# Kernel optimization log

Hardware: AMD Instinct MI355X
Metric: run time of the kernel (lower is better)

Reference implementation:

```python
import jax, jax.numpy as jnp
import numpy as np

N, E, IN_FEATS, HID, HEADS = 50000, 800000, 256, 32, 8
NEG_SLOPE = 0.2


def _init_params(key):
    ks = jax.random.split(key, 12)
    def lin(k, fi, fo):
        return jax.random.normal(k, (fi, fo), jnp.float32) * (1.0 / np.sqrt(fi))
    p = {}
    # layer 0: in_feats -> HID x HEADS
    p['W0'] = lin(ks[0], IN_FEATS, HEADS * HID)
    p['al0'] = jax.random.normal(ks[1], (HEADS, HID), jnp.float32) * 0.1
    p['ar0'] = jax.random.normal(ks[2], (HEADS, HID), jnp.float32) * 0.1
    p['b0'] = jnp.zeros((HEADS * HID,), jnp.float32)
    # layer 1: HID*HEADS -> HID x HEADS
    p['W1'] = lin(ks[3], HEADS * HID, HEADS * HID)
    p['al1'] = jax.random.normal(ks[4], (HEADS, HID), jnp.float32) * 0.1
    p['ar1'] = jax.random.normal(ks[5], (HEADS, HID), jnp.float32) * 0.1
    p['b1'] = jnp.zeros((HEADS * HID,), jnp.float32)
    # layer 2 (final): HID*HEADS -> HID x 1 head, no activation
    p['W2'] = lin(ks[6], HEADS * HID, HID)
    p['al2'] = jax.random.normal(ks[7], (1, HID), jnp.float32) * 0.1
    p['ar2'] = jax.random.normal(ks[8], (1, HID), jnp.float32) * 0.1
    p['b2'] = jnp.zeros((HID,), jnp.float32)
    return p


def setup_inputs() -> dict:
    key = jax.random.key(0)
    k1, k2, k3, kp = jax.random.split(key, 4)
    inp = {
        'features': jax.random.normal(k1, (N, IN_FEATS), jnp.float32),
        'src': jax.random.randint(k2, (E,), 0, N, jnp.int32),
        'dst': jax.random.randint(k3, (E,), 0, N, jnp.int32),
    }
    inp.update(_init_params(kp))
    return inp


def _gat_layer(x, src, dst, W, al, ar, b, heads, act):
    n = x.shape[0]
    d = W.shape[1] // heads
    feat = (x @ W).reshape(n, heads, d)           # [N,H,D]
    el = jnp.sum(feat * al, axis=-1)              # [N,H]
    er = jnp.sum(feat * ar, axis=-1)              # [N,H]
    e = jax.nn.leaky_relu(el[src] + er[dst], NEG_SLOPE)   # [E,H]
    # segment softmax over destination neighborhoods
    emax = jax.ops.segment_max(e, dst, num_segments=n)
    ex = jnp.exp(e - emax[dst])
    denom = jax.ops.segment_sum(ex, dst, num_segments=n)
    a = ex / (denom[dst] + 1e-9)                  # [E,H]
    msg = feat[src] * a[:, :, None]               # [E,H,D]
    out = jax.ops.segment_sum(msg, dst, num_segments=n)   # [N,H,D]
    out = out + b.reshape(1, heads, d)
    return act(out) if act is not None else out


def reference(features, src, dst, W0, al0, ar0, b0, W1, al1, ar1, b1, W2, al2, ar2, b2):
    h = _gat_layer(features, src, dst, W0, al0, ar0, b0, HEADS, jax.nn.elu)
    h = h.reshape(h.shape[0], -1)
    h = _gat_layer(h, src, dst, W1, al1, ar1, b1, HEADS, jax.nn.elu)
    h = h.reshape(h.shape[0], -1)
    h = _gat_layer(h, src, dst, W2, al2, ar2, b2, 1, None)   # [N,1,D]
    return h.mean(axis=1)                                    # [N,D]
```

## Files before the change

### kernel.cpp

```cpp
#include <hip/hip_runtime.h>

typedef unsigned short u16;
typedef unsigned int   u32;
typedef __attribute__((ext_vector_type(8))) short  short8;
typedef __attribute__((ext_vector_type(4))) float  f32x4;
typedef __attribute__((ext_vector_type(2))) float  f32x2;
typedef __attribute__((ext_vector_type(2))) unsigned int u32v2;
typedef __attribute__((ext_vector_type(4))) unsigned int u32v4;

#define NN 50000
#define NE 800000

__device__ __forceinline__ float bf2f(u16 b) { return __uint_as_float(((u32)b) << 16); }
__device__ __forceinline__ float bflo(u32 p) { return __uint_as_float(p << 16); }
__device__ __forceinline__ float bfhi(u32 p) { return __uint_as_float(p & 0xffff0000u); }
__device__ __forceinline__ u16 f2bf(float f) {
    u32 u = __float_as_uint(f);
    u32 r = u + 0x7fffu + ((u >> 16) & 1u);
    return (u16)(r >> 16);
}
__device__ __forceinline__ float lexp(float v) {
    v = fmaxf(v, 0.2f * v);
    return __expf(fminf(v, 60.f));
}

struct DetectArgs { const u32* p[13]; int nw[13]; };

__global__ __launch_bounds__(256) void k_detect(DetectArgs a, int* flags) {
    __shared__ int sh[256], sz[256];
    int j = blockIdx.x;
    const u32* x = a.p[j];
    int n = a.nw[j];
    int t = threadIdx.x;
    int hits = 0, nz = 0;
    for (int i = t; i < n; i += 256) {
        u32 w = x[i];
        if (w) {
            ++nz;
            u32 e = (w >> 7) & 0xffu;
            if (e >= 100 && e <= 150) ++hits;
        }
    }
    sh[t] = hits; sz[t] = nz;
    __syncthreads();
    for (int ofs = 128; ofs > 0; ofs >>= 1) {
        if (t < ofs) { sh[t] += sh[t + ofs]; sz[t] += sz[t + ofs]; }
        __syncthreads();
    }
    if (t == 0) flags[j] = (sz[0] == 0) ? 2 : ((sh[0] * 2 >= sz[0]) ? 0 : 1);
}

struct ConvArgs { const void* s[9]; float* d[9]; int n[9]; int fi[9]; };

__global__ void k_convert(ConvArgs a, const int* __restrict__ flags) {
    int j = blockIdx.y;
    int i = blockIdx.x * 256 + threadIdx.x;
    if (i >= a.n[j]) return;
    int fl = flags[a.fi[j]];
    float v = 0.f;
    if (fl == 1) v = ((const float*)a.s[j])[i];
    else if (fl == 0) v = bf2f(((const u16*)a.s[j])[i]);
    a.d[j][i] = v;
}

__global__ void k_wpack(const void* __restrict__ Wsrc, const int* __restrict__ flags,
                        int fidx, int N, u16* __restrict__ Wp, int nchunks) {
    int id = blockIdx.x * 256 + threadIdx.x;
    if (id >= nchunks) return;
    int L = id & 63, kt = (id >> 6) & 7, nt = id >> 9;
    int col = nt * 16 + (L & 15);
    int krow = kt * 32 + ((L >> 4) & 3) * 8;
    bool isf32 = (flags[fidx] == 1);
#pragma unroll
    for (int j = 0; j < 8; ++j) {
        int s = (krow + j) * N + col;
        Wp[id * 8 + j] = isf32 ? f2bf(((const float*)Wsrc)[s]) : ((const u16*)Wsrc)[s];
    }
}

__global__ void k_hist(const int* __restrict__ dst, int* __restrict__ deg, int E) {
    int e = blockIdx.x * 256 + threadIdx.x;
    if (e < E) atomicAdd(&deg[dst[e]], 1);
}

__global__ __launch_bounds__(256) void k_scan_partial(const int* __restrict__ deg,
                                                      int* __restrict__ bsum, int n) {
    __shared__ int red[256];
    int t = threadIdx.x;
    int i = blockIdx.x * 256 + t;
    red[t] = (i < n) ? deg[i] : 0;
    __syncthreads();
    for (int ofs = 128; ofs > 0; ofs >>= 1) {
        if (t < ofs) red[t] += red[t + ofs];
        __syncthreads();
    }
    if (t == 0) bsum[blockIdx.x] = red[0];
}

__global__ __launch_bounds__(256) void k_scan_bsum(int* __restrict__ bsum, int nb) {
    __shared__ int s[256];
    int t = threadIdx.x;
    int v = (t < nb) ? bsum[t] : 0;
    s[t] = v;
    __syncthreads();
    for (int ofs = 1; ofs < 256; ofs <<= 1) {
        int x = (t >= ofs) ? s[t - ofs] : 0;
        __syncthreads();
        s[t] += x;
        __syncthreads();
    }
    if (t < nb) bsum[t] = s[t] - v;
}

__global__ __launch_bounds__(256) void k_scan_final(const int* __restrict__ deg,
                                                    const int* __restrict__ bsum,
                                                    int* __restrict__ rowptr,
                                                    int* __restrict__ cursor, int n) {
    __shared__ int s[256];
    int t = threadIdx.x;
    int i = blockIdx.x * 256 + t;
    int v = (i < n) ? deg[i] : 0;
    s[t] = v;
    __syncthreads();
    for (int ofs = 1; ofs < 256; ofs <<= 1) {
        int x = (t >= ofs) ? s[t - ofs] : 0;
        __syncthreads();
        s[t] += x;
        __syncthreads();
    }
    int excl = bsum[blockIdx.x] + s[t] - v;
    if (i < n) {
        rowptr[i] = excl;
        cursor[i] = excl;
        if (i == n - 1) rowptr[n] = excl + v;
    }
}

__global__ void k_scatter(const int* __restrict__ src, const int* __restrict__ dst,
                          int* __restrict__ cursor, int* __restrict__ csr_src, int E) {
    int e = blockIdx.x * 256 + threadIdx.x;
    if (e >= E) return;
    int p = atomicAdd(&cursor[dst[e]], 1);
    csr_src[p] = src[e];
}

__global__ __launch_bounds__(256) void k_gemm_mfma(const void* __restrict__ Xv,
                                                   const int* __restrict__ xflag,
                                                   const u16* __restrict__ Wp,
                                                   u16* __restrict__ OUT, int nrows) {
    __shared__ u16 As[64 * 256];
    const int t = threadIdx.x;
    const int w = t >> 6, L = t & 63;
    const int quad = (L >> 4) & 3;
    const int r0 = blockIdx.x * 64;
    const int nb = blockIdx.y * 8;
    const bool xf32 = (xflag != nullptr) && (*xflag == 1);

    short8* Asv = (short8*)As;
    short8 zero = {0, 0, 0, 0, 0, 0, 0, 0};
#pragma unroll
    for (int i = 0; i < 8; ++i) {
        int g = i * 256 + t;
        int row = g >> 5, cc = g & 31;
        int r = r0 + row;
        short8 val = zero;
        if (r < nrows) {
            if (xf32) {
                const f32x4* Xf4 = (const f32x4*)Xv;
                f32x4 lo = Xf4[(size_t)r * 64 + cc * 2];
                f32x4 hi = Xf4[(size_t)r * 64 + cc * 2 + 1];
                val[0] = (short)f2bf(lo[0]); val[1] = (short)f2bf(lo[1]);
                val[2] = (short)f2bf(lo[2]); val[3] = (short)f2bf(lo[3]);
                val[4] = (short)f2bf(hi[0]); val[5] = (short)f2bf(hi[1]);
                val[6] = (short)f2bf(hi[2]); val[7] = (short)f2bf(hi[3]);
            } else {
                val = ((const short8*)Xv)[(size_t)r * 32 + cc];
            }
        }
        Asv[cc * 64 + (row ^ (cc & 7))] = val;
    }

    const short8* Wv = (const short8*)Wp;
    short8 bf[2][8];
#pragma unroll
    for (int jn = 0; jn < 2; ++jn) {
        int nt = nb + w + jn * 4;
#pragma unroll
        for (int kt = 0; kt < 8; ++kt) bf[jn][kt] = Wv[(nt * 8 + kt) * 64 + L];
    }
    __syncthreads();

    f32x4 acc[4][2];
#pragma unroll
    for (int mi = 0; mi < 4; ++mi)
#pragma unroll
        for (int jn = 0; jn < 2; ++jn) acc[mi][jn] = (f32x4){0.f, 0.f, 0.f, 0.f};

#pragma unroll
    for (int kt = 0; kt < 8; ++kt) {
        const int ccr = kt * 4 + quad;
#pragma unroll
        for (int mi = 0; mi < 4; ++mi) {
            short8 af = Asv[ccr * 64 + ((mi * 16 + (L & 15)) ^ (ccr & 7))];
            acc[mi][0] = __builtin_amdgcn_mfma_f32_16x16x32_bf16(af, bf[0][kt], acc[mi][0], 0, 0, 0);
            acc[mi][1] = __builtin_amdgcn_mfma_f32_16x16x32_bf16(af, bf[1][kt], acc[mi][1], 0, 0, 0);
        }
    }

    const int colbase = blockIdx.y * 128;
#pragma unroll
    for (int mi = 0; mi < 4; ++mi) {
        int rb = r0 + mi * 16 + quad * 4;
#pragma unroll
        for (int jn = 0; jn < 2; ++jn) {
            int c = colbase + (w + jn * 4) * 16 + (L & 15);
#pragma unroll
            for (int reg = 0; reg < 4; ++reg) {
                int r = rb + reg;
                if (r < nrows) OUT[(size_t)r * 256 + c] = f2bf(acc[mi][jn][reg]);
            }
        }
    }
}

__global__ __launch_bounds__(256) void k_gemm_mfma32(const u16* __restrict__ Xb,
                                                     const u16* __restrict__ Wp,
                                                     u16* __restrict__ OUT, int nrows) {
    __shared__ u16 As[128 * 256];
    const int t = threadIdx.x;
    const int w = t >> 6, L = t & 63;
    const int quad = (L >> 4) & 3;
    const int r0 = blockIdx.x * 128;
    const int mh = (w >> 1) * 64, nt = w & 1;

    const short8* Xv = (const short8*)Xb;
    short8* Asv = (short8*)As;
    short8 zero = {0, 0, 0, 0, 0, 0, 0, 0};
#pragma unroll
    for (int i = 0; i < 16; ++i) {
        int g = i * 256 + t;
        int row = g >> 5, cc = g & 31;
        int r = r0 + row;
        Asv[cc * 128 + (row ^ (cc & 7))] = (r < nrows) ? Xv[(size_t)r * 32 + cc] : zero;
    }

    const short8* Wv = (const short8*)Wp;
    short8 bf[8];
#pragma unroll
    for (int kt = 0; kt < 8; ++kt) bf[kt] = Wv[(nt * 8 + kt) * 64 + L];
    __syncthreads();

    f32x4 acc[4];
#pragma unroll
    for (int mi = 0; mi < 4; ++mi) acc[mi] = (f32x4){0.f, 0.f, 0.f, 0.f};

#pragma unroll
    for (int kt = 0; kt < 8; ++kt) {
        const int ccr = kt * 4 + quad;
#pragma unroll
        for (int mi = 0; mi < 4; ++mi) {
            short8 af = Asv[ccr * 128 + ((mh + mi * 16 + (L & 15)) ^ (ccr & 7))];
            acc[mi] = __builtin_amdgcn_mfma_f32_16x16x32_bf16(af, bf[kt], acc[mi], 0, 0, 0);
        }
    }

#pragma unroll
    for (int mi = 0; mi < 4; ++mi) {
        int rb = r0 + mh + mi * 16 + quad * 4;
        int c = nt * 16 + (L & 15);
#pragma unroll
        for (int reg = 0; reg < 4; ++reg) {
            int r = rb + reg;
            if (r < nrows) OUT[(size_t)r * 32 + c] = f2bf(acc[mi][reg]);
        }
    }
}

__global__ void k_elr8(const u16* __restrict__ featb, const float* __restrict__ al,
                       const float* __restrict__ ar, float* __restrict__ el,
                       float* __restrict__ er, int n) {
    int idx = blockIdx.x * 256 + threadIdx.x;
    if (idx >= n * 8) return;
    int node = idx >> 3, h = idx & 7;
    const u32v4* fu = (const u32v4*)((const u32*)featb + (size_t)node * 128 + h * 16);
    const float* A = al + h * 32;
    const float* B = ar + h * 32;
    float sl = 0.f, sr = 0.f;
#pragma unroll
    for (int j = 0; j < 4; ++j) {
        u32v4 w4 = fu[j];
#pragma unroll
        for (int k = 0; k < 4; ++k) {
            u32 w = (k == 0) ? w4.x : (k == 1) ? w4.y : (k == 2) ? w4.z : w4.w;
            float f0 = bflo(w), f1 = bfhi(w);
            int c = j * 8 + k * 2;
            sl += f0 * A[c] + f1 * A[c + 1];
            sr += f0 * B[c] + f1 * B[c + 1];
        }
    }
    el[idx] = sl;
    er[idx] = sr;
}

__global__ void k_elr1(const u16* __restrict__ featb, const float* __restrict__ al,
                       const float* __restrict__ ar, float* __restrict__ el,
                       float* __restrict__ er, int n) {
    int node = blockIdx.x * 256 + threadIdx.x;
    if (node >= n) return;
    const u32v4* fu = (const u32v4*)((const u32*)featb + (size_t)node * 16);
    float sl = 0.f, sr = 0.f;
#pragma unroll
    for (int j = 0; j < 4; ++j) {
        u32v4 w4 = fu[j];
#pragma unroll
        for (int k = 0; k < 4; ++k) {
            u32 w = (k == 0) ? w4.x : (k == 1) ? w4.y : (k == 2) ? w4.z : w4.w;
            float f0 = bflo(w), f1 = bfhi(w);
            int c = j * 8 + k * 2;
            sl += f0 * al[c] + f1 * al[c + 1];
            sr += f0 * ar[c] + f1 * ar[c + 1];
        }
    }
    el[node] = sl;
    er[node] = sr;
}

__global__ __launch_bounds__(256) void k_gather8(const int* __restrict__ rowptr,
                                                 const int* __restrict__ csr_src,
                                                 const float* __restrict__ el,
                                                 const float* __restrict__ er,
                                                 const u32v2* __restrict__ featb4,
                                                 const float* __restrict__ bias,
                                                 u32v2* __restrict__ xout4) {
    __shared__ __align__(16) float sAL[4][2][64];
    __shared__ __align__(16) int   sSL[4][2][8];
    const int t = threadIdx.x;
    const int wv = t >> 6;
    const int q = t & 63;
    const int d = blockIdx.x * 4 + wv;
    const int eL = q >> 3, hL = q & 7;
    const int b = rowptr[d], e = rowptr[d + 1];
    const int deg = e - b;
    const int nch = (deg + 7) >> 3;
    const float erA = er[d * 8 + hL];

    float (*AL)[64] = sAL[wv];
    int (*SL)[8] = sSL[wv];

    float a0 = 0.f, a1 = 0.f, a2 = 0.f, a3 = 0.f;
    float partial = 0.f;

    u32v2 fw[8], fw2[8];
    int csrP = 0, ncP = 0;
    float elP = 0.f;

    if (nch > 0) {
        const int nc0 = deg < 8 ? deg : 8;
        const int i0 = eL < nc0 ? eL : nc0 - 1;
        const int s0 = csr_src[b + i0];
        if (nch > 1) {
            const int r1 = deg - 8;
            ncP = r1 < 8 ? r1 : 8;
            const int i1 = eL < ncP ? eL : ncP - 1;
            csrP = csr_src[b + 8 + i1];
        }
        const float el0 = el[s0 * 8 + hL];
        if (hL == 0) SL[0][eL] = s0;
        const int4 sv0 = *(const int4*)&SL[0][0];
        const int4 sv1 = *(const int4*)&SL[0][4];
        fw[0] = featb4[sv0.x * 64 + q];
        fw[1] = featb4[sv0.y * 64 + q];
        fw[2] = featb4[sv0.z * 64 + q];
        fw[3] = featb4[sv0.w * 64 + q];
        fw[4] = featb4[sv1.x * 64 + q];
        fw[5] = featb4[sv1.y * 64 + q];
        fw[6] = featb4[sv1.z * 64 + q];
        fw[7] = featb4[sv1.w * 64 + q];
        const float ex0 = (eL < nc0) ? lexp(el0 + erA) : 0.f;
        partial += ex0;
        AL[0][hL * 8 + eL] = ex0;
        if (nch > 1) elP = el[csrP * 8 + hL];
    }

    for (int c = 0; c < nch; ++c) {
        const int cur = c & 1, nxt = cur ^ 1;

        int csrF = 0, ncF = 0;
        if (c + 2 < nch) {
            const int r2 = deg - (c + 2) * 8;
            ncF = r2 < 8 ? r2 : 8;
            const int i2 = eL < ncF ? eL : ncF - 1;
            csrF = csr_src[b + (c + 2) * 8 + i2];
        }

        if (c + 1 < nch) {
            if (hL == 0) SL[nxt][eL] = csrP;
            const int4 sv0 = *(const int4*)&SL[nxt][0];
            const int4 sv1 = *(const int4*)&SL[nxt][4];
            fw2[0] = featb4[sv0.x * 64 + q];
            fw2[1] = featb4[sv0.y * 64 + q];
            fw2[2] = featb4[sv0.z * 64 + q];
            fw2[3] = featb4[sv0.w * 64 + q];
            fw2[4] = featb4[sv1.x * 64 + q];
            fw2[5] = featb4[sv1.y * 64 + q];
            fw2[6] = featb4[sv1.z * 64 + q];
            fw2[7] = featb4[sv1.w * 64 + q];
            const float exN = (eL < ncP) ? lexp(elP + erA) : 0.f;
            partial += exN;
            AL[nxt][hL * 8 + eL] = exN;
        }

        const int h8 = (q >> 3) * 8;
        const f32x4 A0 = *(const f32x4*)&AL[cur][h8];
        const f32x4 A1 = *(const f32x4*)&AL[cur][h8 + 4];

        if (c + 2 < nch) elP = el[csrF * 8 + hL];

#define GAT_EDGE(i, axv) { const u32v2 w_ = fw[i]; \
        a0 += bflo(w_.x) * (axv); a1 += bfhi(w_.x) * (axv); \
        a2 += bflo(w_.y) * (axv); a3 += bfhi(w_.y) * (axv); }
        GAT_EDGE(0, A0[0]) GAT_EDGE(1, A0[1]) GAT_EDGE(2, A0[2]) GAT_EDGE(3, A0[3])
        GAT_EDGE(4, A1[0]) GAT_EDGE(5, A1[1]) GAT_EDGE(6, A1[2]) GAT_EDGE(7, A1[3])
#undef GAT_EDGE

#pragma unroll
        for (int i = 0; i < 8; ++i) fw[i] = fw2[i];
        csrP = csrF;
        ncP = ncF;
    }

    float v = partial;
    v += __shfl_xor(v, 8);
    v += __shfl_xor(v, 16);
    v += __shfl_xor(v, 32);
    const float ssd = __shfl(v, q >> 3);

    const float rd = 1.f / (ssd + 1e-9f);
    const float4 bb = *(const float4*)&bias[4 * q];
    float v0 = a0 * rd + bb.x;
    float v1 = a1 * rd + bb.y;
    float v2 = a2 * rd + bb.z;
    float v3 = a3 * rd + bb.w;
    v0 = v0 > 0.f ? v0 : expm1f(v0);
    v1 = v1 > 0.f ? v1 : expm1f(v1);
    v2 = v2 > 0.f ? v2 : expm1f(v2);
    v3 = v3 > 0.f ? v3 : expm1f(v3);
    u32v2 o;
    o.x = (u32)f2bf(v0) | ((u32)f2bf(v1) << 16);
    o.y = (u32)f2bf(v2) | ((u32)f2bf(v3) << 16);
    xout4[(size_t)d * 64 + q] = o;
}

__global__ __launch_bounds__(256) void k_gather1(const int* __restrict__ rowptr,
                                                 const int* __restrict__ csr_src,
                                                 const float* __restrict__ el,
                                                 const float* __restrict__ er,
                                                 const u32* __restrict__ featb2,
                                                 const float* __restrict__ bias,
                                                 void* __restrict__ out,
                                                 const int* __restrict__ flag, int n) {
    int t = threadIdx.x;
    int d = blockIdx.x * 16 + (t >> 4);
    int q = t & 15;
    if (d >= n) return;
    int b = rowptr[d], e = rowptr[d + 1];
    float erd = er[d];
    float a0 = 0.f, a1 = 0.f, ssum = 0.f;
    int p = b;
    for (; p + 4 <= e; p += 4) {
        int s0 = csr_src[p], s1 = csr_src[p + 1], s2 = csr_src[p + 2], s3 = csr_src[p + 3];
        float e0 = lexp(el[s0] + erd);
        float e1 = lexp(el[s1] + erd);
        float e2 = lexp(el[s2] + erd);
        float e3 = lexp(el[s3] + erd);
        u32 w0 = featb2[(size_t)s0 * 16 + q];
        u32 w1 = featb2[(size_t)s1 * 16 + q];
        u32 w2 = featb2[(size_t)s2 * 16 + q];
        u32 w3 = featb2[(size_t)s3 * 16 + q];
        a0 += bflo(w0) * e0; a1 += bfhi(w0) * e0;
        a0 += bflo(w1) * e1; a1 += bfhi(w1) * e1;
        a0 += bflo(w2) * e2; a1 += bfhi(w2) * e2;
        a0 += bflo(w3) * e3; a1 += bfhi(w3) * e3;
        ssum += (e0 + e1) + (e2 + e3);
    }
    for (; p < e; ++p) {
        int s = csr_src[p];
        float ev = lexp(el[s] + erd);
        u32 w = featb2[(size_t)s * 16 + q];
        a0 += bflo(w) * ev;
        a1 += bfhi(w) * ev;
        ssum += ev;
    }
    float rd = 1.f / (ssum + 1e-9f);
    float v0 = a0 * rd + bias[2 * q];
    float v1 = a1 * rd + bias[2 * q + 1];
    if (*flag == 1) {
        f32x2 o = {v0, v1};
        ((f32x2*)out)[(size_t)d * 16 + q] = o;
    } else {
        ((u32*)out)[(size_t)d * 16 + q] = (u32)f2bf(v0) | ((u32)f2bf(v1) << 16);
    }
}

extern "C" void kernel_launch(void* const* d_in, const int* in_sizes, int n_in,
                              void* d_out, int out_size, void* d_ws, size_t ws_size,
                              hipStream_t stream) {
    const void* features = d_in[0];
    const int* src = (const int*)d_in[1];
    const int* dst = (const int*)d_in[2];

    char* ws = (char*)d_ws;
    size_t off = 0;
    auto carve = [&](size_t bytes) -> void* {
        void* p = ws + off;
        off = (off + bytes + 255) & ~(size_t)255;
        return p;
    };
    int*   flags = (int*)carve(64);
    float* pconv = (float*)carve(2048 * 4);
    u16*   Wp0 = (u16*)carve(65536 * 2);
    u16*   Wp1 = (u16*)carve(65536 * 2);
    u16*   Wp2 = (u16*)carve(8192 * 2);
    u16*   Xb    = (u16*)carve((size_t)NN * 256 * 2);
    u16*   featb = (u16*)carve((size_t)NN * 256 * 2);
    float* el   = (float*)carve((size_t)NN * 8 * 4);
    float* er   = (float*)carve((size_t)NN * 8 * 4);
    int*   deg     = (int*)carve((size_t)NN * 4);
    int*   cursor  = (int*)carve((size_t)NN * 4);
    int*   rowptr  = (int*)carve((size_t)(NN + 1) * 4);
    int*   bsum    = (int*)carve(256 * 4);
    int*   csr_src = (int*)carve((size_t)NE * 4);
    if (off > ws_size) return;

    const int N = NN, E = NE;
    const int nscan = (N + 255) / 256;

    DetectArgs da;
    const int din_idx[13] = {0, 3, 4, 5, 6, 7, 8, 9, 10, 11, 12, 13, 14};
    for (int j = 0; j < 13; ++j) {
        da.p[j] = (const u32*)d_in[din_idx[j]];
        int nw = in_sizes[din_idx[j]] / 2;
        da.nw[j] = nw > 512 ? 512 : nw;
    }
    k_detect<<<13, 256, 0, stream>>>(da, flags);

    ConvArgs ca;
    const int psl[9] = {4, 5, 6, 8, 9, 10, 12, 13, 14};
    const int pfl[9] = {2, 3, 4, 6, 7, 8, 10, 11, 12};
    float* dsts[9];
    {
        size_t o = 0;
        for (int j = 0; j < 9; ++j) {
            dsts[j] = pconv + o;
            o += (size_t)in_sizes[psl[j]];
        }
    }
    for (int j = 0; j < 9; ++j) {
        ca.s[j] = d_in[psl[j]];
        ca.d[j] = dsts[j];
        ca.n[j] = in_sizes[psl[j]];
        ca.fi[j] = pfl[j];
    }
    k_convert<<<dim3(1, 9), 256, 0, stream>>>(ca, flags);
    float* al0f = dsts[0]; float* ar0f = dsts[1]; float* b0f = dsts[2];
    float* al1f = dsts[3]; float* ar1f = dsts[4]; float* b1f = dsts[5];
    float* al2f = dsts[6]; float* ar2f = dsts[7]; float* b2f = dsts[8];

    k_wpack<<<32, 256, 0, stream>>>(d_in[3],  flags, 1, 256, Wp0, 8192);
    k_wpack<<<32, 256, 0, stream>>>(d_in[7],  flags, 5, 256, Wp1, 8192);
    k_wpack<<<4,  256, 0, stream>>>(d_in[11], flags, 9, 32,  Wp2, 1024);

    hipMemsetAsync(deg, 0, (size_t)N * 4, stream);
    k_hist<<<(E + 255) / 256, 256, 0, stream>>>(dst, deg, E);
    k_scan_partial<<<nscan, 256, 0, stream>>>(deg, bsum, N);
    k_scan_bsum<<<1, 256, 0, stream>>>(bsum, nscan);
    k_scan_final<<<nscan, 256, 0, stream>>>(deg, bsum, rowptr, cursor, N);
    k_scatter<<<(E + 255) / 256, 256, 0, stream>>>(src, dst, cursor, csr_src, E);

    const dim3 ggrid((N + 63) / 64, 2);

    k_gemm_mfma<<<ggrid, 256, 0, stream>>>(features, flags, Wp0, featb, N);
    k_elr8<<<(N * 8 + 255) / 256, 256, 0, stream>>>(featb, al0f, ar0f, el, er, N);
    k_gather8<<<N / 4, 256, 0, stream>>>(rowptr, csr_src, el, er,
                                         (const u32v2*)featb, b0f, (u32v2*)Xb);

    k_gemm_mfma<<<ggrid, 256, 0, stream>>>(Xb, nullptr, Wp1, featb, N);
    k_elr8<<<(N * 8 + 255) / 256, 256, 0, stream>>>(featb, al1f, ar1f, el, er, N);
    k_gather8<<<N / 4, 256, 0, stream>>>(rowptr, csr_src, el, er,
                                         (const u32v2*)featb, b1f, (u32v2*)Xb);

    k_gemm_mfma32<<<(N + 127) / 128, 256, 0, stream>>>(Xb, Wp2, featb, N);
    k_elr1<<<(N + 255) / 256, 256, 0, stream>>>(featb, al2f, ar2f, el, er, N);
    k_gather1<<<(N + 15) / 16, 256, 0, stream>>>(rowptr, csr_src, el, er,
                                                 (const u32*)featb, b2f,
                                                 d_out, flags, N);
}
```

Measured before the change: 447.3 us.

## Merge prep kernels into one launch and widen GEMM blocks to full width

Combines the dtype-detect, parameter-convert and weight-pack kernels into a single prep kernel in which each block runs its own format detection, removing four launches and the flag dependency between them. Separately, the layer-0/1 GEMM now uses 512-thread blocks that cover all 256 output columns, so each 64-row A tile is loaded into shared memory once instead of twice. The cost is redundant detect work in every prep block and a larger block that may lower occupancy.

Result: faster. 418.4 us (-6.5%).

```diff
diff --git a/kernel.cpp b/kernel.cpp
--- a/kernel.cpp
+++ b/kernel.cpp
@@ -24,13 +24,7 @@
     return __expf(fminf(v, 60.f));
 }
 
-struct DetectArgs { const u32* p[13]; int nw[13]; };
-
-__global__ __launch_bounds__(256) void k_detect(DetectArgs a, int* flags) {
-    __shared__ int sh[256], sz[256];
-    int j = blockIdx.x;
-    const u32* x = a.p[j];
-    int n = a.nw[j];
+__device__ __forceinline__ int block_detect(const u32* x, int n, int* sh, int* sz) {
     int t = threadIdx.x;
     int hits = 0, nz = 0;
     for (int i = t; i < n; i += 256) {
@@ -47,34 +41,54 @@
         if (t < ofs) { sh[t] += sh[t + ofs]; sz[t] += sz[t + ofs]; }
         __syncthreads();
     }
-    if (t == 0) flags[j] = (sz[0] == 0) ? 2 : ((sh[0] * 2 >= sz[0]) ? 0 : 1);
-}
-
-struct ConvArgs { const void* s[9]; float* d[9]; int n[9]; int fi[9]; };
-
-__global__ void k_convert(ConvArgs a, const int* __restrict__ flags) {
-    int j = blockIdx.y;
-    int i = blockIdx.x * 256 + threadIdx.x;
-    if (i >= a.n[j]) return;
-    int fl = flags[a.fi[j]];
-    float v = 0.f;
-    if (fl == 1) v = ((const float*)a.s[j])[i];
-    else if (fl == 0) v = bf2f(((const u16*)a.s[j])[i]);
-    a.d[j][i] = v;
-}
-
-__global__ void k_wpack(const void* __restrict__ Wsrc, const int* __restrict__ flags,
-                        int fidx, int N, u16* __restrict__ Wp, int nchunks) {
-    int id = blockIdx.x * 256 + threadIdx.x;
-    if (id >= nchunks) return;
-    int L = id & 63, kt = (id >> 6) & 7, nt = id >> 9;
-    int col = nt * 16 + (L & 15);
-    int krow = kt * 32 + ((L >> 4) & 3) * 8;
-    bool isf32 = (flags[fidx] == 1);
-#pragma unroll
-    for (int j = 0; j < 8; ++j) {
-        int s = (krow + j) * N + col;
-        Wp[id * 8 + j] = isf32 ? f2bf(((const float*)Wsrc)[s]) : ((const u16*)Wsrc)[s];
+    return (sz[0] == 0) ? 2 : ((sh[0] * 2 >= sz[0]) ? 0 : 1);
+}
+
+struct PrepArgs {
+    const u32* dp[13]; int dnw[13];
+    const void* cs[9]; float* cd[9]; int cn[9];
+    const void* wsrc[3]; u16* wdst[3]; int wN[3]; int wchunks[3];
+};
+
+__global__ __launch_bounds__(256) void k_prep(PrepArgs a, int* flags) {
+    __shared__ int sh[256], sz[256];
+    const int bid = blockIdx.x;
+    const int t = threadIdx.x;
+    if (bid < 13) {
+        int f = block_detect(a.dp[bid], a.dnw[bid], sh, sz);
+        if (t == 0) flags[bid] = f;
+    } else if (bid < 22) {
+        const int j = bid - 13;
+        int nw = a.cn[j] / 2; if (nw > 512) nw = 512;
+        const int fl = block_detect((const u32*)a.cs[j], nw, sh, sz);
+        if (t < a.cn[j]) {
+            float v = 0.f;
+            if (fl == 1) v = ((const float*)a.cs[j])[t];
+            else if (fl == 0) v = bf2f(((const u16*)a.cs[j])[t]);
+            a.cd[j][t] = v;
+        }
+    } else {
+        int wj, base;
+        if (bid < 54)      { wj = 0; base = 22; }
+        else if (bid < 86) { wj = 1; base = 54; }
+        else               { wj = 2; base = 86; }
+        const void* Wsrc = a.wsrc[wj];
+        const int fl = block_detect((const u32*)Wsrc, 512, sh, sz);
+        const int id = (bid - base) * 256 + t;
+        if (id < a.wchunks[wj]) {
+            const int L = id & 63, kt = (id >> 6) & 7, nt = id >> 9;
+            const int col = nt * 16 + (L & 15);
+            const int krow = kt * 32 + ((L >> 4) & 3) * 8;
+            const bool isf32 = (fl == 1);
+            const int N = a.wN[wj];
+            u16* Wp = a.wdst[wj];
+#pragma unroll
+            for (int j2 = 0; j2 < 8; ++j2) {
+                int s = (krow + j2) * N + col;
+                Wp[id * 8 + j2] = isf32 ? f2bf(((const float*)Wsrc)[s])
+                                        : ((const u16*)Wsrc)[s];
+            }
+        }
     }
 }
 
@@ -144,7 +158,7 @@
     csr_src[p] = src[e];
 }
 
-__global__ __launch_bounds__(256) void k_gemm_mfma(const void* __restrict__ Xv,
+__global__ __launch_bounds__(512) void k_gemm_mfma(const void* __restrict__ Xv,
                                                    const int* __restrict__ xflag,
                                                    const u16* __restrict__ Wp,
                                                    u16* __restrict__ OUT, int nrows) {
@@ -153,14 +167,13 @@
     const int w = t >> 6, L = t & 63;
     const int quad = (L >> 4) & 3;
     const int r0 = blockIdx.x * 64;
-    const int nb = blockIdx.y * 8;
     const bool xf32 = (xflag != nullptr) && (*xflag == 1);
 
     short8* Asv = (short8*)As;
     short8 zero = {0, 0, 0, 0, 0, 0, 0, 0};
 #pragma unroll
-    for (int i = 0; i < 8; ++i) {
-        int g = i * 256 + t;
+    for (int i = 0; i < 4; ++i) {
+        int g = i * 512 + t;
         int row = g >> 5, cc = g & 31;
         int r = r0 + row;
         short8 val = zero;
@@ -184,7 +197,7 @@
     short8 bf[2][8];
 #pragma unroll
     for (int jn = 0; jn < 2; ++jn) {
-        int nt = nb + w + jn * 4;
+        int nt = w + jn * 8;
 #pragma unroll
         for (int kt = 0; kt < 8; ++kt) bf[jn][kt] = Wv[(nt * 8 + kt) * 64 + L];
     }
@@ -207,13 +220,12 @@
         }
     }
 
-    const int colbase = blockIdx.y * 128;
 #pragma unroll
     for (int mi = 0; mi < 4; ++mi) {
         int rb = r0 + mi * 16 + quad * 4;
 #pragma unroll
         for (int jn = 0; jn < 2; ++jn) {
-            int c = colbase + (w + jn * 4) * 16 + (L & 15);
+            int c = (w + jn * 8) * 16 + (L & 15);
 #pragma unroll
             for (int reg = 0; reg < 4; ++reg) {
                 int r = rb + reg;
@@ -535,18 +547,14 @@
     const int N = NN, E = NE;
     const int nscan = (N + 255) / 256;
 
-    DetectArgs da;
+    PrepArgs pa;
     const int din_idx[13] = {0, 3, 4, 5, 6, 7, 8, 9, 10, 11, 12, 13, 14};
     for (int j = 0; j < 13; ++j) {
-        da.p[j] = (const u32*)d_in[din_idx[j]];
+        pa.dp[j] = (const u32*)d_in[din_idx[j]];
         int nw = in_sizes[din_idx[j]] / 2;
-        da.nw[j] = nw > 512 ? 512 : nw;
-    }
-    k_detect<<<13, 256, 0, stream>>>(da, flags);
-
-    ConvArgs ca;
+        pa.dnw[j] = nw > 512 ? 512 : nw;
+    }
     const int psl[9] = {4, 5, 6, 8, 9, 10, 12, 13, 14};
-    const int pfl[9] = {2, 3, 4, 6, 7, 8, 10, 11, 12};
     float* dsts[9];
     {
         size_t o = 0;
@@ -556,19 +564,17 @@
         }
     }
     for (int j = 0; j < 9; ++j) {
-        ca.s[j] = d_in[psl[j]];
-        ca.d[j] = dsts[j];
-        ca.n[j] = in_sizes[psl[j]];
-        ca.fi[j] = pfl[j];
-    }
-    k_convert<<<dim3(1, 9), 256, 0, stream>>>(ca, flags);
+        pa.cs[j] = d_in[psl[j]];
+        pa.cd[j] = dsts[j];
+        pa.cn[j] = in_sizes[psl[j]];
+    }
+    pa.wsrc[0] = d_in[3];  pa.wdst[0] = Wp0; pa.wN[0] = 256; pa.wchunks[0] = 8192;
+    pa.wsrc[1] = d_in[7];  pa.wdst[1] = Wp1; pa.wN[1] = 256; pa.wchunks[1] = 8192;
+    pa.wsrc[2] = d_in[11]; pa.wdst[2] = Wp2; pa.wN[2] = 32;  pa.wchunks[2] = 1024;
+    k_prep<<<90, 256, 0, stream>>>(pa, flags);
     float* al0f = dsts[0]; float* ar0f = dsts[1]; float* b0f = dsts[2];
     float* al1f = dsts[3]; float* ar1f = dsts[4]; float* b1f = dsts[5];
     float* al2f = dsts[6]; float* ar2f = dsts[7]; float* b2f = dsts[8];
-
-    k_wpack<<<32, 256, 0, stream>>>(d_in[3],  flags, 1, 256, Wp0, 8192);
-    k_wpack<<<32, 256, 0, stream>>>(d_in[7],  flags, 5, 256, Wp1, 8192);
-    k_wpack<<<4,  256, 0, stream>>>(d_in[11], flags, 9, 32,  Wp2, 1024);
 
     hipMemsetAsync(deg, 0, (size_t)N * 4, stream);
     k_hist<<<(E + 255) / 256, 256, 0, stream>>>(dst, deg, E);
@@ -577,14 +583,14 @@
     k_scan_final<<<nscan, 256, 0, stream>>>(deg, bsum, rowptr, cursor, N);
     k_scatter<<<(E + 255) / 256, 256, 0, stream>>>(src, dst, cursor, csr_src, E);
 
-    const dim3 ggrid((N + 63) / 64, 2);
-
-    k_gemm_mfma<<<ggrid, 256, 0, stream>>>(features, flags, Wp0, featb, N);
+    const int ggrid = (N + 63) / 64;
+
+    k_gemm_mfma<<<ggrid, 512, 0, stream>>>(features, flags, Wp0, featb, N);
     k_elr8<<<(N * 8 + 255) / 256, 256, 0, stream>>>(featb, al0f, ar0f, el, er, N);
     k_gather8<<<N / 4, 256, 0, stream>>>(rowptr, csr_src, el, er,
                                          (const u32v2*)featb, b0f, (u32v2*)Xb);
 
-    k_gemm_mfma<<<ggrid, 256, 0, stream>>>(Xb, nullptr, Wp1, featb, N);
+    k_gemm_mfma<<<ggrid, 512, 0, stream>>>(Xb, nullptr, Wp1, featb, N);
     k_elr8<<<(N * 8 + 255) / 256, 256, 0, stream>>>(featb, al1f, ar1f, el, er, N);
     k_gather8<<<N / 4, 256, 0, stream>>>(rowptr, csr_src, el, er,
                                          (const u32v2*)featb, b1f, (u32v2*)Xb);
```
